# Kernel tuning notes

Hardware: AMD Instinct MI355X
Metric: run time of the kernel (lower is better)

## Reference

```python
import jax, jax.numpy as jnp
import numpy as np
import math

N_HEADS = 16
D_MODEL = 1024
DK = D_MODEL // N_HEADS
B, S = 2, 2048


def setup_inputs() -> dict:
    key = jax.random.key(0)
    ks = jax.random.split(key, 11)
    scale_in = 1.0 / math.sqrt(D_MODEL)
    scale_o = 1.0 / math.sqrt(N_HEADS * DK)
    return {
        "query": jax.random.normal(ks[0], (B, S, D_MODEL), jnp.float32),
        "key": jax.random.normal(ks[1], (B, S, D_MODEL), jnp.float32),
        "value": jax.random.normal(ks[2], (B, S, D_MODEL), jnp.float32),
        # stacked per-head projection weights [H, d_model, dk], biases [H, dk]
        "Wq": jax.random.normal(ks[3], (N_HEADS, D_MODEL, DK), jnp.float32) * scale_in,
        "bq": jax.random.normal(ks[4], (N_HEADS, DK), jnp.float32) * scale_in,
        "Wk": jax.random.normal(ks[5], (N_HEADS, D_MODEL, DK), jnp.float32) * scale_in,
        "bk": jax.random.normal(ks[6], (N_HEADS, DK), jnp.float32) * scale_in,
        "Wv": jax.random.normal(ks[7], (N_HEADS, D_MODEL, DK), jnp.float32) * scale_in,
        "bv": jax.random.normal(ks[8], (N_HEADS, DK), jnp.float32) * scale_in,
        "Wo": jax.random.normal(ks[9], (N_HEADS * DK, D_MODEL), jnp.float32) * scale_o,
        "bo": jax.random.normal(ks[10], (D_MODEL,), jnp.float32) * scale_o,
    }


def reference(query, key, value, Wq, bq, Wk, bk, Wv, bv, Wo, bo):
    # Per-head linear projections, vectorized over heads: [B,H,S,dk]
    q = jnp.einsum("bsd,hdk->bhsk", query, Wq) + bq[None, :, None, :]
    k = jnp.einsum("bsd,hdk->bhsk", key, Wk) + bk[None, :, None, :]
    v = jnp.einsum("bsd,hdk->bhsk", value, Wv) + bv[None, :, None, :]
    # Scaled dot-product scores [B,H,S,S]
    scores = jnp.einsum("bhsk,bhtk->bhst", q, k) / jnp.sqrt(jnp.asarray(DK, q.dtype))
    # FAITHFUL to source: nn.Softmax(dim=0) -> softmax over the BATCH axis
    attn = jax.nn.softmax(scores, axis=0)
    out = jnp.einsum("bhst,bhtk->bhsk", attn, v)  # [B,H,S,dk]
    # concat heads along feature dim (torch.cat dim=2)
    concat = out.transpose(0, 2, 1, 3).reshape(query.shape[0], query.shape[1], N_HEADS * DK)
    return concat @ Wo + bo
```

## Files before the change

### kernel.cpp

```cpp
#include <hip/hip_runtime.h>
#include <hip/hip_bf16.h>

#define B_ 2
#define S_ 2048
#define D_ 1024
#define H_ 16
#define DK_ 64
#define BS_ (B_ * S_)

typedef unsigned int u32;
typedef unsigned short u16;
typedef __attribute__((ext_vector_type(8))) short bf16x8;
typedef __attribute__((ext_vector_type(4))) float f32x4;

typedef const __attribute__((address_space(1))) void glb_cv;
typedef __attribute__((address_space(3))) void lds_v;

__device__ __forceinline__ void async_cp16(const void* g, void* l) {
    __builtin_amdgcn_global_load_lds((glb_cv*)g, (lds_v*)l, 16, 0, 0);
}

__device__ __forceinline__ float bf2f(u16 v) {
    union { u32 u; float f; } c; c.u = ((u32)v) << 16; return c.f;
}
__device__ __forceinline__ u16 f2bf(float f) {
    union { float f; u32 u; } c; c.f = f;
    u32 u = c.u;
    return (u16)((u + 0x7fffu + ((u >> 16) & 1u)) >> 16);
}
__device__ __forceinline__ u32 pack2(float a, float b) {
    return (u32)f2bf(a) | ((u32)f2bf(b) << 16);
}
__device__ __forceinline__ u32 packtr(float lo, float hi) {
    union { float f; u32 u; } a, b; a.f = lo; b.f = hi;
    return __builtin_amdgcn_perm(b.u, a.u, 0x07060302u);
}
__device__ __forceinline__ int sw64(int r, int c8) { return (((c8) + (r)) & 7) * 8; }

struct PrepArgs {
    const float* W[4]; u16* WT[4];
    const float* X[3]; u16* XB[3];
    float* csums;
};
__global__ __launch_bounds__(256) void prep(PrepArgs a)
{
    const int id = blockIdx.x;
    const int tid = threadIdx.x;
    if (id >= 1024) {
        const int cid = id - 1024;
        const int z = cid >> 11;
        const size_t base = (size_t)(cid & 2047) * 2048 + tid * 8;
        const float* X = a.X[z];
        float4 x0 = *(const float4*)(X + base);
        float4 x1 = *(const float4*)(X + base + 4);
        uint4 o;
        o.x = pack2(x0.x, x0.y); o.y = pack2(x0.z, x0.w);
        o.z = pack2(x1.x, x1.y); o.w = pack2(x1.z, x1.w);
        *(uint4*)(a.XB[z] + base) = o;
        return;
    }
    if (id == 0) {
        float4 zz = {0.f, 0.f, 0.f, 0.f};
        *(float4*)(a.csums + tid * 4) = zz;
    }
    __shared__ __attribute__((aligned(16))) u16 T[64][72];
    const int z = id >> 8;
    const int rem = id & 255;
    const float* W = a.W[z];
    u16* WT = a.WT[z];
    const int headMode = (z < 3) ? 1 : 0;
    const int k0 = (rem >> 4) * 64;
    const int n0 = (rem & 15) * 64;
    const int kr = tid >> 4;
    const int n4 = (tid & 15) * 4;
    #pragma unroll
    for (int pass = 0; pass < 4; ++pass) {
        int kk = k0 + pass * 16 + kr;
        const float* p = headMode
            ? (W + (size_t)((n0 + n4) >> 6) * (1024 * 64) + kk * 64 + ((n0 + n4) & 63))
            : (W + (size_t)kk * 1024 + n0 + n4);
        float4 v = *(const float4*)p;
        int krel = pass * 16 + kr;
        T[n4 + 0][krel] = f2bf(v.x);
        T[n4 + 1][krel] = f2bf(v.y);
        T[n4 + 2][krel] = f2bf(v.z);
        T[n4 + 3][krel] = f2bf(v.w);
    }
    __syncthreads();
    const int nr = tid >> 2;
    const int kq = (tid & 3) * 16;
    uint4 o0 = *(const uint4*)&T[nr][kq];
    uint4 o1 = *(const uint4*)&T[nr][kq + 8];
    u16* q = WT + (size_t)(n0 + nr) * 1024 + k0 + kq;
    *(uint4*)q = o0;
    *(uint4*)(q + 8) = o1;
}

__global__ __launch_bounds__(256) void vprep(
    const u16* __restrict__ Vb, u16* __restrict__ VT, float* __restrict__ csums)
{
    __shared__ __attribute__((aligned(16))) u16 T[64][72];
    __shared__ float red[256];
    const int tid = threadIdx.x;
    const int t0 = blockIdx.x * 64;
    const int bh = blockIdx.y;
    const int b = bh >> 4, h = bh & 15;
    const int tr = tid >> 4;
    const int d4 = (tid & 15) * 4;
    #pragma unroll
    for (int pass = 0; pass < 4; ++pass) {
        int tt = t0 + pass * 16 + tr;
        const u16* p = Vb + (size_t)(b * S_ + tt) * 1024 + h * 64 + d4;
        u32 a = *(const u32*)p;
        u32 c = *(const u32*)(p + 2);
        int trel = pass * 16 + tr;
        T[d4 + 0][trel] = (u16)a;
        T[d4 + 1][trel] = (u16)(a >> 16);
        T[d4 + 2][trel] = (u16)c;
        T[d4 + 3][trel] = (u16)(c >> 16);
    }
    __syncthreads();
    const int dr = tid >> 2;
    const int tq = (tid & 3) * 16;
    uint4 o0 = *(const uint4*)&T[dr][tq];
    uint4 o1 = *(const uint4*)&T[dr][tq + 8];
    u16* q = VT + ((size_t)bh * 64 + dr) * 2048 + t0 + tq;
    *(uint4*)q = o0;
    *(uint4*)(q + 8) = o1;

    if (b == 1) {
        const int dk = tid & 63, part = tid >> 6;
        float s = 0.f;
        #pragma unroll
        for (int t = 0; t < 16; ++t) s += bf2f(T[dk][part * 16 + t]);
        red[tid] = s;
        __syncthreads();
        if (tid < 64)
            atomicAdd(&csums[h * 64 + tid],
                      red[tid] + red[tid + 64] + red[tid + 128] + red[tid + 192]);
    }
}

struct ProjArgs {
    const u16* X[3];
    const u16* W[3];
    const float* bias[3];
    u16* Y[3];
};
__global__ __launch_bounds__(256) void proj3(ProjArgs pa)
{
    __shared__ __attribute__((aligned(16))) u16 As[128][32];
    __shared__ __attribute__((aligned(16))) u16 Bs[128][32];
    const int z = blockIdx.z;
    const u16* X = pa.X[z];
    const u16* WT = pa.W[z];
    const float* bias = pa.bias[z];
    u16* Y = pa.Y[z];
    const int neg = (z == 1);

    const int tid = threadIdx.x;
    const int lane = tid & 63;
    const int wave = tid >> 6;
    const int quad = lane >> 4;
    const int l16 = lane & 15;
    const int m0 = blockIdx.x * 128;
    const int n0 = blockIdx.y * 128;
    const int wm = (wave & 1) * 64, wn = (wave >> 1) * 64;

    f32x4 acc[4][4] = {};

    for (int k0 = 0; k0 < 1024; k0 += 32) {
        __syncthreads();
        #pragma unroll
        for (int call = 0; call < 2; ++call) {
            const int c = tid + call * 256;
            const int row = c >> 2, cc = (c & 3) * 8;
            char* la = (char*)&As[0][0] + (size_t)(c & ~63) * 16;
            async_cp16(X + (size_t)(m0 + row) * 1024 + k0 + cc, la);
            char* lb = (char*)&Bs[0][0] + (size_t)(c & ~63) * 16;
            async_cp16(WT + (size_t)(n0 + row) * 1024 + k0 + cc, lb);
        }
        __syncthreads();

        bf16x8 af[4], bfr[4];
        #pragma unroll
        for (int mt = 0; mt < 4; ++mt)
            af[mt] = *(const bf16x8*)&As[wm + mt * 16 + l16][quad * 8];
        #pragma unroll
        for (int nt = 0; nt < 4; ++nt)
            bfr[nt] = *(const bf16x8*)&Bs[wn + nt * 16 + l16][quad * 8];
        #pragma unroll
        for (int mt = 0; mt < 4; ++mt)
            #pragma unroll
            for (int nt = 0; nt < 4; ++nt)
                acc[mt][nt] = __builtin_amdgcn_mfma_f32_16x16x32_bf16(
                    af[mt], bfr[nt], acc[mt][nt], 0, 0, 0);
    }

    #pragma unroll
    for (int nt = 0; nt < 4; ++nt) {
        const int col = n0 + wn + nt * 16 + l16;
        const float bv = bias[col];
        #pragma unroll
        for (int mt = 0; mt < 4; ++mt) {
            #pragma unroll
            for (int r = 0; r < 4; ++r) {
                const int row = m0 + wm + mt * 16 + quad * 4 + r;
                float v = acc[mt][nt][r] + bv;
                if (neg && row >= 2048) v = -v;
                Y[(size_t)row * 1024 + col] = f2bf(v);
            }
        }
    }
}

__global__ __launch_bounds__(256) void gemm_out(
    const u16* __restrict__ X, const u16* __restrict__ WT,
    const float* __restrict__ bias, float* __restrict__ Y)
{
    __shared__ __attribute__((aligned(16))) u16 As[128][32];
    __shared__ __attribute__((aligned(16))) u16 Bs[64][32];
    const int tid = threadIdx.x;
    const int lane = tid & 63;
    const int wave = tid >> 6;
    const int quad = lane >> 4;
    const int l16 = lane & 15;
    const int m0 = blockIdx.x * 128;
    const int n0 = blockIdx.y * 64;
    const int wm = (wave & 1) * 64, wn = (wave >> 1) * 32;

    f32x4 acc[4][2] = {};

    for (int k0 = 0; k0 < 1024; k0 += 32) {
        __syncthreads();
        #pragma unroll
        for (int call = 0; call < 2; ++call) {
            const int c = tid + call * 256;
            const int row = c >> 2, cc = (c & 3) * 8;
            char* la = (char*)&As[0][0] + (size_t)(c & ~63) * 16;
            async_cp16(X + (size_t)(m0 + row) * 1024 + k0 + cc, la);
        }
        {
            const int c = tid;
            const int row = c >> 2, cc = (c & 3) * 8;
            char* lb = (char*)&Bs[0][0] + (size_t)(c & ~63) * 16;
            async_cp16(WT + (size_t)(n0 + row) * 1024 + k0 + cc, lb);
        }
        __syncthreads();

        bf16x8 af[4], bfr[2];
        #pragma unroll
        for (int mt = 0; mt < 4; ++mt)
            af[mt] = *(const bf16x8*)&As[wm + mt * 16 + l16][quad * 8];
        #pragma unroll
        for (int nt = 0; nt < 2; ++nt)
            bfr[nt] = *(const bf16x8*)&Bs[wn + nt * 16 + l16][quad * 8];
        #pragma unroll
        for (int mt = 0; mt < 4; ++mt)
            #pragma unroll
            for (int nt = 0; nt < 2; ++nt)
                acc[mt][nt] = __builtin_amdgcn_mfma_f32_16x16x32_bf16(
                    af[mt], bfr[nt], acc[mt][nt], 0, 0, 0);
    }

    #pragma unroll
    for (int nt = 0; nt < 2; ++nt) {
        const int col = n0 + wn + nt * 16 + l16;
        const float bv = bias[col];
        #pragma unroll
        for (int mt = 0; mt < 4; ++mt) {
            #pragma unroll
            for (int r = 0; r < 4; ++r) {
                const int row = m0 + wm + mt * 16 + quad * 4 + r;
                Y[(size_t)row * 1024 + col] = acc[mt][nt][r] + bv;
            }
        }
    }
}

__global__ __launch_bounds__(256) void attn_mfma(
    const u16* __restrict__ Qb, const u16* __restrict__ Kb,
    const u16* __restrict__ VT, const float* __restrict__ csums,
    u16* __restrict__ Cc)
{
    __shared__ __attribute__((aligned(16))) u16 Ks[2][64][64];
    __shared__ __attribute__((aligned(16))) u16 Vs[2][64][64];
    __shared__ __attribute__((aligned(16))) u16 Ps[64][64];

    const int id = blockIdx.x;
    const int xcd = id & 7, j = id >> 3;
    const int h = xcd + 8 * (j >> 5);
    const int s0 = (j & 31) * 64;

    const int tid = threadIdx.x;
    const int lane = tid & 63;
    const int wave = tid >> 6;
    const int quad = lane >> 4;
    const int l16 = lane & 15;
    const int sw = wave * 16;

    const int r_ = tid >> 2;
    const int cq = (tid & 3) * 16;
    const int cq8 = (tid & 3) * 2;

    bf16x8 qf[2][2];
    #pragma unroll
    for (int b = 0; b < 2; ++b)
        #pragma unroll
        for (int ks = 0; ks < 2; ++ks)
            qf[b][ks] = *(const bf16x8*)(Qb + (size_t)(b * S_ + s0 + sw + l16) * 1024
                                          + h * 64 + ks * 32 + quad * 8);

    f32x4 O0[4] = {}, T1[4] = {};

    for (int t0 = 0; t0 < S_; t0 += 64) {
        __syncthreads();
        #pragma unroll
        for (int b = 0; b < 2; ++b) {
            const u16* pk = Kb + (size_t)(b * S_ + t0 + r_) * 1024 + h * 64 + cq;
            *(uint4*)&Ks[b][r_][sw64(r_, cq8)]     = *(const uint4*)pk;
            *(uint4*)&Ks[b][r_][sw64(r_, cq8 + 1)] = *(const uint4*)(pk + 8);
            const u16* pv = VT + ((size_t)(b * H_ + h) * 64 + r_) * 2048 + t0 + cq;
            *(uint4*)&Vs[b][r_][sw64(r_, cq8)]     = *(const uint4*)pv;
            *(uint4*)&Vs[b][r_][sw64(r_, cq8 + 1)] = *(const uint4*)(pv + 8);
        }
        __syncthreads();

        f32x4 dacc[4] = {};
        #pragma unroll
        for (int mt = 0; mt < 4; ++mt) {
            const int kr = mt * 16 + l16;
            #pragma unroll
            for (int ks = 0; ks < 2; ++ks) {
                bf16x8 k0f = *(const bf16x8*)&Ks[0][kr][sw64(kr, ks * 4 + quad)];
                dacc[mt] = __builtin_amdgcn_mfma_f32_16x16x32_bf16(k0f, qf[0][ks], dacc[mt], 0, 0, 0);
                bf16x8 k1f = *(const bf16x8*)&Ks[1][kr][sw64(kr, ks * 4 + quad)];
                dacc[mt] = __builtin_amdgcn_mfma_f32_16x16x32_bf16(k1f, qf[1][ks], dacc[mt], 0, 0, 0);
            }
        }
        const int pr = sw + l16;
        #pragma unroll
        for (int mt = 0; mt < 4; ++mt) {
            float p[4];
            #pragma unroll
            for (int r = 0; r < 4; ++r) {
                float e = __expf(dacc[mt][r] * -0.125f);
                p[r] = __builtin_amdgcn_rcpf(1.0f + e);
            }
            uint2 w;
            w.x = packtr(p[0], p[1]);
            w.y = packtr(p[2], p[3]);
            const int c8 = 2 * mt + (quad >> 1);
            *(uint2*)&Ps[pr][sw64(pr, c8) + (quad & 1) * 4] = w;
        }
        bf16x8 pf0 = *(const bf16x8*)&Ps[pr][sw64(pr, quad)];
        bf16x8 pf1 = *(const bf16x8*)&Ps[pr][sw64(pr, 4 + quad)];
        #pragma unroll
        for (int nt = 0; nt < 4; ++nt) {
            const int vr = nt * 16 + l16;
            bf16x8 v00 = *(const bf16x8*)&Vs[0][vr][sw64(vr, quad)];
            bf16x8 v01 = *(const bf16x8*)&Vs[0][vr][sw64(vr, 4 + quad)];
            O0[nt] = __builtin_amdgcn_mfma_f32_16x16x32_bf16(pf0, v00, O0[nt], 0, 0, 0);
            O0[nt] = __builtin_amdgcn_mfma_f32_16x16x32_bf16(pf1, v01, O0[nt], 0, 0, 0);
            bf16x8 v10 = *(const bf16x8*)&Vs[1][vr][sw64(vr, quad)];
            bf16x8 v11 = *(const bf16x8*)&Vs[1][vr][sw64(vr, 4 + quad)];
            T1[nt] = __builtin_amdgcn_mfma_f32_16x16x32_bf16(pf0, v10, T1[nt], 0, 0, 0);
            T1[nt] = __builtin_amdgcn_mfma_f32_16x16x32_bf16(pf1, v11, T1[nt], 0, 0, 0);
        }
    }

    #pragma unroll
    for (int nt = 0; nt < 4; ++nt) {
        const int dk = nt * 16 + l16;
        const float cs1 = csums[h * 64 + dk];
        #pragma unroll
        for (int r = 0; r < 4; ++r) {
            const int s = s0 + sw + quad * 4 + r;
            Cc[(size_t)(0 * S_ + s) * 1024 + h * 64 + dk] = f2bf(O0[nt][r]);
            Cc[(size_t)(1 * S_ + s) * 1024 + h * 64 + dk] = f2bf(cs1 - T1[nt][r]);
        }
    }
}

extern "C" void kernel_launch(void* const* d_in, const int* in_sizes, int n_in,
                              void* d_out, int out_size, void* d_ws, size_t ws_size,
                              hipStream_t stream) {
    const float* q  = (const float*)d_in[0];
    const float* k  = (const float*)d_in[1];
    const float* v  = (const float*)d_in[2];
    const float* Wq = (const float*)d_in[3];
    const float* bq = (const float*)d_in[4];
    const float* Wk = (const float*)d_in[5];
    const float* bk = (const float*)d_in[6];
    const float* Wv = (const float*)d_in[7];
    const float* bv = (const float*)d_in[8];
    const float* Wo = (const float*)d_in[9];
    const float* bo = (const float*)d_in[10];

    char* ws = (char*)d_ws;
    const size_t MB = 1024 * 1024;
    u16* Cc  = (u16*)(ws);
    u16* Xq  = (u16*)(ws);
    u16* WqT = (u16*)(ws + 8  * MB);
    u16* WkT = (u16*)(ws + 10 * MB);
    u16* WvT = (u16*)(ws + 12 * MB);
    u16* WoT = (u16*)(ws + 14 * MB);
    u16* Qp  = (u16*)(ws + 16 * MB);
    u16* Kp  = (u16*)(ws + 24 * MB);
    u16* Vp  = (u16*)(ws + 32 * MB);
    u16* VTv = (u16*)(ws + 40 * MB);
    u16* Xk  = (u16*)(ws + 40 * MB);
    u16* Xv  = (u16*)(ws + 48 * MB);
    float* csums = (float*)d_out;

    dim3 blk(256);

    PrepArgs pr;
    pr.W[0] = Wq; pr.W[1] = Wk; pr.W[2] = Wv; pr.W[3] = Wo;
    pr.WT[0] = WqT; pr.WT[1] = WkT; pr.WT[2] = WvT; pr.WT[3] = WoT;
    pr.X[0] = q; pr.X[1] = k; pr.X[2] = v;
    pr.XB[0] = Xq; pr.XB[1] = Xk; pr.XB[2] = Xv;
    pr.csums = csums;
    prep<<<dim3(1024 + 6144), blk, 0, stream>>>(pr);

    ProjArgs pa;
    pa.X[0] = Xq; pa.X[1] = Xk; pa.X[2] = Xv;
    pa.W[0] = WqT; pa.W[1] = WkT; pa.W[2] = WvT;
    pa.bias[0] = bq; pa.bias[1] = bk; pa.bias[2] = bv;
    pa.Y[0] = Qp; pa.Y[1] = Kp; pa.Y[2] = Vp;
    proj3<<<dim3(32, 8, 3), blk, 0, stream>>>(pa);

    vprep<<<dim3(32, 32), blk, 0, stream>>>(Vp, VTv, csums);
    attn_mfma<<<dim3(512), blk, 0, stream>>>(Qp, Kp, VTv, csums, Cc);
    gemm_out<<<dim3(32, 16), blk, 0, stream>>>(Cc, WoT, bo, (float*)d_out);
}
```

Before: 233.7 us.

## Split attention key range across blocks, double-buffer K/V, merge partials in output GEMM

The attention kernel now handles 128 query rows per block and splits the key dimension into two halves across blocks. K/V tiles are staged asynchronously into double-buffered LDS, with MFMA priority hints. Each half writes its own partial output, and the column sums of V are computed inside attention instead of through atomics in vprep. The output GEMM loads both partials, adds them, applies the csum correction for batch 1, and packs the result into LDS. This trades asynchronous A loads in gemm_out for synchronous loads plus extra arithmetic, and it doubles the partial-output traffic, in exchange for more parallelism and overlap in attention.

```diff
diff --git a/kernel.cpp b/kernel.cpp
--- a/kernel.cpp
+++ b/kernel.cpp
@@ -40,7 +40,6 @@
 struct PrepArgs {
     const float* W[4]; u16* WT[4];
     const float* X[3]; u16* XB[3];
-    float* csums;
 };
 __global__ __launch_bounds__(256) void prep(PrepArgs a)
 {
@@ -58,10 +57,6 @@
         o.z = pack2(x1.x, x1.y); o.w = pack2(x1.z, x1.w);
         *(uint4*)(a.XB[z] + base) = o;
         return;
-    }
-    if (id == 0) {
-        float4 zz = {0.f, 0.f, 0.f, 0.f};
-        *(float4*)(a.csums + tid * 4) = zz;
     }
     __shared__ __attribute__((aligned(16))) u16 T[64][72];
     const int z = id >> 8;
@@ -97,10 +92,9 @@
 }
 
 __global__ __launch_bounds__(256) void vprep(
-    const u16* __restrict__ Vb, u16* __restrict__ VT, float* __restrict__ csums)
+    const u16* __restrict__ Vb, u16* __restrict__ VT)
 {
     __shared__ __attribute__((aligned(16))) u16 T[64][72];
-    __shared__ float red[256];
     const int tid = threadIdx.x;
     const int t0 = blockIdx.x * 64;
     const int bh = blockIdx.y;
@@ -127,18 +121,6 @@
     u16* q = VT + ((size_t)bh * 64 + dr) * 2048 + t0 + tq;
     *(uint4*)q = o0;
     *(uint4*)(q + 8) = o1;
-
-    if (b == 1) {
-        const int dk = tid & 63, part = tid >> 6;
-        float s = 0.f;
-        #pragma unroll
-        for (int t = 0; t < 16; ++t) s += bf2f(T[dk][part * 16 + t]);
-        red[tid] = s;
-        __syncthreads();
-        if (tid < 64)
-            atomicAdd(&csums[h * 64 + tid],
-                      red[tid] + red[tid + 64] + red[tid + 128] + red[tid + 192]);
-    }
 }
 
 struct ProjArgs {
@@ -215,8 +197,10 @@
 }
 
 __global__ __launch_bounds__(256) void gemm_out(
-    const u16* __restrict__ X, const u16* __restrict__ WT,
-    const float* __restrict__ bias, float* __restrict__ Y)
+    const u16* __restrict__ P0, const u16* __restrict__ P1,
+    const float* __restrict__ csP,
+    const u16* __restrict__ WT, const float* __restrict__ bias,
+    float* __restrict__ Y)
 {
     __shared__ __attribute__((aligned(16))) u16 As[128][32];
     __shared__ __attribute__((aligned(16))) u16 Bs[64][32];
@@ -229,23 +213,51 @@
     const int n0 = blockIdx.y * 64;
     const int wm = (wave & 1) * 64, wn = (wave >> 1) * 32;
 
+    const int arow = tid >> 1;
+    const int acol = (tid & 1) * 16;
+    const size_t abase = (size_t)(m0 + arow) * 1024;
+    const bool hiB = (m0 >= 2048);
+
     f32x4 acc[4][2] = {};
 
     for (int k0 = 0; k0 < 1024; k0 += 32) {
         __syncthreads();
-        #pragma unroll
-        for (int call = 0; call < 2; ++call) {
-            const int c = tid + call * 256;
-            const int row = c >> 2, cc = (c & 3) * 8;
-            char* la = (char*)&As[0][0] + (size_t)(c & ~63) * 16;
-            async_cp16(X + (size_t)(m0 + row) * 1024 + k0 + cc, la);
-        }
         {
             const int c = tid;
             const int row = c >> 2, cc = (c & 3) * 8;
             char* lb = (char*)&Bs[0][0] + (size_t)(c & ~63) * 16;
             async_cp16(WT + (size_t)(n0 + row) * 1024 + k0 + cc, lb);
         }
+        const size_t off = abase + k0 + acol;
+        bf16x8 a0 = *(const bf16x8*)(P0 + off);
+        bf16x8 a1 = *(const bf16x8*)(P0 + off + 8);
+        bf16x8 b0 = *(const bf16x8*)(P1 + off);
+        bf16x8 b1 = *(const bf16x8*)(P1 + off + 8);
+        float va[16];
+        #pragma unroll
+        for (int jj = 0; jj < 8; ++jj) {
+            va[jj]     = bf2f((u16)a0[jj]) + bf2f((u16)b0[jj]);
+            va[8 + jj] = bf2f((u16)a1[jj]) + bf2f((u16)b1[jj]);
+        }
+        if (hiB) {
+            #pragma unroll
+            for (int g = 0; g < 4; ++g) {
+                const int cb = k0 + acol + g * 4;
+                float4 c0 = *(const float4*)(csP + cb);
+                float4 c1 = *(const float4*)(csP + 1024 + cb);
+                va[g * 4 + 0] = (c0.x + c1.x) - va[g * 4 + 0];
+                va[g * 4 + 1] = (c0.y + c1.y) - va[g * 4 + 1];
+                va[g * 4 + 2] = (c0.z + c1.z) - va[g * 4 + 2];
+                va[g * 4 + 3] = (c0.w + c1.w) - va[g * 4 + 3];
+            }
+        }
+        uint4 w0, w1;
+        w0.x = pack2(va[0], va[1]);   w0.y = pack2(va[2], va[3]);
+        w0.z = pack2(va[4], va[5]);   w0.w = pack2(va[6], va[7]);
+        w1.x = pack2(va[8], va[9]);   w1.y = pack2(va[10], va[11]);
+        w1.z = pack2(va[12], va[13]); w1.w = pack2(va[14], va[15]);
+        *(uint4*)&As[arow][acol] = w0;
+        *(uint4*)&As[arow][acol + 8] = w1;
         __syncthreads();
 
         bf16x8 af[4], bfr[2];
@@ -280,105 +292,159 @@
 
 __global__ __launch_bounds__(256) void attn_mfma(
     const u16* __restrict__ Qb, const u16* __restrict__ Kb,
-    const u16* __restrict__ VT, const float* __restrict__ csums,
-    u16* __restrict__ Cc)
+    const u16* __restrict__ VT, float* __restrict__ csP,
+    u16* __restrict__ P0, u16* __restrict__ P1)
 {
-    __shared__ __attribute__((aligned(16))) u16 Ks[2][64][64];
-    __shared__ __attribute__((aligned(16))) u16 Vs[2][64][64];
-    __shared__ __attribute__((aligned(16))) u16 Ps[64][64];
+    __shared__ __attribute__((aligned(16))) u16 Ks[2][2][64][64];
+    __shared__ __attribute__((aligned(16))) u16 Vs[2][2][64][64];
+    __shared__ __attribute__((aligned(16))) u16 Ps[128][64];
 
     const int id = blockIdx.x;
-    const int xcd = id & 7, j = id >> 3;
-    const int h = xcd + 8 * (j >> 5);
-    const int s0 = (j & 31) * 64;
+    const int xcd = id & 7;
+    const int rj = id >> 3;
+    const int h = xcd * 2 + (rj >> 5);
+    const int half = (rj >> 4) & 1;
+    const int st = rj & 15;
+    const int s0 = st * 128;
+    const int tbase = half * 1024;
+    u16* Pout = half ? P1 : P0;
 
     const int tid = threadIdx.x;
     const int lane = tid & 63;
     const int wave = tid >> 6;
     const int quad = lane >> 4;
     const int l16 = lane & 15;
-    const int sw = wave * 16;
-
-    const int r_ = tid >> 2;
-    const int cq = (tid & 3) * 16;
-    const int cq8 = (tid & 3) * 2;
-
-    bf16x8 qf[2][2];
+    const int sr8 = lane >> 3;
+    const int sc8 = lane & 7;
+
+    auto stage = [&](int buf, int t0) {
+        #pragma unroll
+        for (int c = 0; c < 4; ++c) {
+            const int kc = c * 4 + wave;
+            const int bb = kc >> 3, row0 = (kc & 7) * 8;
+            const int rr = row0 + sr8;
+            const int cg = (sc8 - rr) & 7;
+            async_cp16(Kb + (size_t)(bb * S_ + tbase + t0 + rr) * 1024 + h * 64 + cg * 8,
+                       &Ks[buf][bb][row0][0]);
+            async_cp16(VT + ((size_t)(bb * H_ + h) * 64 + rr) * 2048 + tbase + t0 + cg * 8,
+                       &Vs[buf][bb][row0][0]);
+        }
+    };
+
+    bf16x8 qf[2][2][2];
     #pragma unroll
-    for (int b = 0; b < 2; ++b)
-        #pragma unroll
-        for (int ks = 0; ks < 2; ++ks)
-            qf[b][ks] = *(const bf16x8*)(Qb + (size_t)(b * S_ + s0 + sw + l16) * 1024
-                                          + h * 64 + ks * 32 + quad * 8);
-
-    f32x4 O0[4] = {}, T1[4] = {};
-
-    for (int t0 = 0; t0 < S_; t0 += 64) {
-        __syncthreads();
-        #pragma unroll
-        for (int b = 0; b < 2; ++b) {
-            const u16* pk = Kb + (size_t)(b * S_ + t0 + r_) * 1024 + h * 64 + cq;
-            *(uint4*)&Ks[b][r_][sw64(r_, cq8)]     = *(const uint4*)pk;
-            *(uint4*)&Ks[b][r_][sw64(r_, cq8 + 1)] = *(const uint4*)(pk + 8);
-            const u16* pv = VT + ((size_t)(b * H_ + h) * 64 + r_) * 2048 + t0 + cq;
-            *(uint4*)&Vs[b][r_][sw64(r_, cq8)]     = *(const uint4*)pv;
-            *(uint4*)&Vs[b][r_][sw64(r_, cq8 + 1)] = *(const uint4*)(pv + 8);
-        }
-        __syncthreads();
-
-        f32x4 dacc[4] = {};
+    for (int sg = 0; sg < 2; ++sg)
+        #pragma unroll
+        for (int b = 0; b < 2; ++b)
+            #pragma unroll
+            for (int ks = 0; ks < 2; ++ks)
+                qf[sg][b][ks] = *(const bf16x8*)(Qb
+                    + (size_t)(b * S_ + s0 + wave * 32 + sg * 16 + l16) * 1024
+                    + h * 64 + ks * 32 + quad * 8);
+
+    f32x4 O0[2][4] = {}, T1[2][4] = {};
+    float cacc = 0.f;
+
+    stage(0, 0);
+    __syncthreads();
+    int cur = 0;
+    for (int t0 = 0; t0 < 1024; t0 += 64) {
+        if (t0 + 64 < 1024) stage(cur ^ 1, t0 + 64);
+
+        f32x4 dacc[2][4] = {};
+        __builtin_amdgcn_s_setprio(1);
         #pragma unroll
         for (int mt = 0; mt < 4; ++mt) {
             const int kr = mt * 16 + l16;
             #pragma unroll
             for (int ks = 0; ks < 2; ++ks) {
-                bf16x8 k0f = *(const bf16x8*)&Ks[0][kr][sw64(kr, ks * 4 + quad)];
-                dacc[mt] = __builtin_amdgcn_mfma_f32_16x16x32_bf16(k0f, qf[0][ks], dacc[mt], 0, 0, 0);
-                bf16x8 k1f = *(const bf16x8*)&Ks[1][kr][sw64(kr, ks * 4 + quad)];
-                dacc[mt] = __builtin_amdgcn_mfma_f32_16x16x32_bf16(k1f, qf[1][ks], dacc[mt], 0, 0, 0);
-            }
-        }
-        const int pr = sw + l16;
-        #pragma unroll
-        for (int mt = 0; mt < 4; ++mt) {
-            float p[4];
-            #pragma unroll
-            for (int r = 0; r < 4; ++r) {
-                float e = __expf(dacc[mt][r] * -0.125f);
-                p[r] = __builtin_amdgcn_rcpf(1.0f + e);
-            }
-            uint2 w;
-            w.x = packtr(p[0], p[1]);
-            w.y = packtr(p[2], p[3]);
-            const int c8 = 2 * mt + (quad >> 1);
-            *(uint2*)&Ps[pr][sw64(pr, c8) + (quad & 1) * 4] = w;
-        }
-        bf16x8 pf0 = *(const bf16x8*)&Ps[pr][sw64(pr, quad)];
-        bf16x8 pf1 = *(const bf16x8*)&Ps[pr][sw64(pr, 4 + quad)];
+                bf16x8 k0f = *(const bf16x8*)&Ks[cur][0][kr][sw64(kr, ks * 4 + quad)];
+                bf16x8 k1f = *(const bf16x8*)&Ks[cur][1][kr][sw64(kr, ks * 4 + quad)];
+                #pragma unroll
+                for (int sg = 0; sg < 2; ++sg) {
+                    dacc[sg][mt] = __builtin_amdgcn_mfma_f32_16x16x32_bf16(
+                        k0f, qf[sg][0][ks], dacc[sg][mt], 0, 0, 0);
+                    dacc[sg][mt] = __builtin_amdgcn_mfma_f32_16x16x32_bf16(
+                        k1f, qf[sg][1][ks], dacc[sg][mt], 0, 0, 0);
+                }
+            }
+        }
+        __builtin_amdgcn_s_setprio(0);
+
+        #pragma unroll
+        for (int sg = 0; sg < 2; ++sg) {
+            const int pr = wave * 32 + sg * 16 + l16;
+            #pragma unroll
+            for (int mt = 0; mt < 4; ++mt) {
+                float p[4];
+                #pragma unroll
+                for (int rr = 0; rr < 4; ++rr) {
+                    float e = __expf(dacc[sg][mt][rr] * -0.125f);
+                    p[rr] = __builtin_amdgcn_rcpf(1.0f + e);
+                }
+                uint2 w;
+                w.x = packtr(p[0], p[1]);
+                w.y = packtr(p[2], p[3]);
+                const int c8 = 2 * mt + (quad >> 1);
+                *(uint2*)&Ps[pr][sw64(pr, c8) + (quad & 1) * 4] = w;
+            }
+        }
+
+        if (st == 0) {
+            const int dk = tid >> 2, tp = tid & 3;
+            bf16x8 vA = *(const bf16x8*)&Vs[cur][1][dk][sw64(dk, tp * 2)];
+            bf16x8 vB = *(const bf16x8*)&Vs[cur][1][dk][sw64(dk, tp * 2 + 1)];
+            #pragma unroll
+            for (int jj = 0; jj < 8; ++jj)
+                cacc += bf2f((u16)vA[jj]) + bf2f((u16)vB[jj]);
+        }
+
+        bf16x8 pf[2][2];
+        #pragma unroll
+        for (int sg = 0; sg < 2; ++sg) {
+            const int pr = wave * 32 + sg * 16 + l16;
+            pf[sg][0] = *(const bf16x8*)&Ps[pr][sw64(pr, quad)];
+            pf[sg][1] = *(const bf16x8*)&Ps[pr][sw64(pr, 4 + quad)];
+        }
+        __builtin_amdgcn_s_setprio(1);
         #pragma unroll
         for (int nt = 0; nt < 4; ++nt) {
             const int vr = nt * 16 + l16;
-            bf16x8 v00 = *(const bf16x8*)&Vs[0][vr][sw64(vr, quad)];
-            bf16x8 v01 = *(const bf16x8*)&Vs[0][vr][sw64(vr, 4 + quad)];
-            O0[nt] = __builtin_amdgcn_mfma_f32_16x16x32_bf16(pf0, v00, O0[nt], 0, 0, 0);
-            O0[nt] = __builtin_amdgcn_mfma_f32_16x16x32_bf16(pf1, v01, O0[nt], 0, 0, 0);
-            bf16x8 v10 = *(const bf16x8*)&Vs[1][vr][sw64(vr, quad)];
-            bf16x8 v11 = *(const bf16x8*)&Vs[1][vr][sw64(vr, 4 + quad)];
-            T1[nt] = __builtin_amdgcn_mfma_f32_16x16x32_bf16(pf0, v10, T1[nt], 0, 0, 0);
-            T1[nt] = __builtin_amdgcn_mfma_f32_16x16x32_bf16(pf1, v11, T1[nt], 0, 0, 0);
-        }
+            bf16x8 v00 = *(const bf16x8*)&Vs[cur][0][vr][sw64(vr, quad)];
+            bf16x8 v01 = *(const bf16x8*)&Vs[cur][0][vr][sw64(vr, 4 + quad)];
+            bf16x8 v10 = *(const bf16x8*)&Vs[cur][1][vr][sw64(vr, quad)];
+            bf16x8 v11 = *(const bf16x8*)&Vs[cur][1][vr][sw64(vr, 4 + quad)];
+            #pragma unroll
+            for (int sg = 0; sg < 2; ++sg) {
+                O0[sg][nt] = __builtin_amdgcn_mfma_f32_16x16x32_bf16(pf[sg][0], v00, O0[sg][nt], 0, 0, 0);
+                O0[sg][nt] = __builtin_amdgcn_mfma_f32_16x16x32_bf16(pf[sg][1], v01, O0[sg][nt], 0, 0, 0);
+                T1[sg][nt] = __builtin_amdgcn_mfma_f32_16x16x32_bf16(pf[sg][0], v10, T1[sg][nt], 0, 0, 0);
+                T1[sg][nt] = __builtin_amdgcn_mfma_f32_16x16x32_bf16(pf[sg][1], v11, T1[sg][nt], 0, 0, 0);
+            }
+        }
+        __builtin_amdgcn_s_setprio(0);
+        __syncthreads();
+        cur ^= 1;
     }
 
     #pragma unroll
-    for (int nt = 0; nt < 4; ++nt) {
-        const int dk = nt * 16 + l16;
-        const float cs1 = csums[h * 64 + dk];
-        #pragma unroll
-        for (int r = 0; r < 4; ++r) {
-            const int s = s0 + sw + quad * 4 + r;
-            Cc[(size_t)(0 * S_ + s) * 1024 + h * 64 + dk] = f2bf(O0[nt][r]);
-            Cc[(size_t)(1 * S_ + s) * 1024 + h * 64 + dk] = f2bf(cs1 - T1[nt][r]);
-        }
+    for (int sg = 0; sg < 2; ++sg)
+        #pragma unroll
+        for (int nt = 0; nt < 4; ++nt) {
+            const int dk = nt * 16 + l16;
+            #pragma unroll
+            for (int rr = 0; rr < 4; ++rr) {
+                const int s = s0 + wave * 32 + sg * 16 + quad * 4 + rr;
+                Pout[(size_t)(0 * S_ + s) * 1024 + h * 64 + dk] = f2bf(O0[sg][nt][rr]);
+                Pout[(size_t)(1 * S_ + s) * 1024 + h * 64 + dk] = f2bf(T1[sg][nt][rr]);
+            }
+        }
+
+    if (st == 0) {
+        cacc += __shfl_xor(cacc, 1);
+        cacc += __shfl_xor(cacc, 2);
+        if ((tid & 3) == 0)
+            csP[half * 1024 + h * 64 + (tid >> 2)] = cacc;
     }
 }
 
@@ -399,8 +465,8 @@
 
     char* ws = (char*)d_ws;
     const size_t MB = 1024 * 1024;
-    u16* Cc  = (u16*)(ws);
     u16* Xq  = (u16*)(ws);
+    float* csP = (float*)(ws);
     u16* WqT = (u16*)(ws + 8  * MB);
     u16* WkT = (u16*)(ws + 10 * MB);
     u16* WvT = (u16*)(ws + 12 * MB);
@@ -408,10 +474,11 @@
     u16* Qp  = (u16*)(ws + 16 * MB);
     u16* Kp  = (u16*)(ws + 24 * MB);
     u16* Vp  = (u16*)(ws + 32 * MB);
+    u16* Pa  = (u16*)(ws + 32 * MB);
     u16* VTv = (u16*)(ws + 40 * MB);
     u16* Xk  = (u16*)(ws + 40 * MB);
     u16* Xv  = (u16*)(ws + 48 * MB);
-    float* csums = (float*)d_out;
+    u16* Pb  = (u16*)(ws + 48 * MB);
 
     dim3 blk(256);
 
@@ -420,7 +487,6 @@
     pr.WT[0] = WqT; pr.WT[1] = WkT; pr.WT[2] = WvT; pr.WT[3] = WoT;
     pr.X[0] = q; pr.X[1] = k; pr.X[2] = v;
     pr.XB[0] = Xq; pr.XB[1] = Xk; pr.XB[2] = Xv;
-    pr.csums = csums;
     prep<<<dim3(1024 + 6144), blk, 0, stream>>>(pr);
 
     ProjArgs pa;
@@ -430,7 +496,7 @@
     pa.Y[0] = Qp; pa.Y[1] = Kp; pa.Y[2] = Vp;
     proj3<<<dim3(32, 8, 3), blk, 0, stream>>>(pa);
 
-    vprep<<<dim3(32, 32), blk, 0, stream>>>(Vp, VTv, csums);
-    attn_mfma<<<dim3(512), blk, 0, stream>>>(Qp, Kp, VTv, csums, Cc);
-    gemm_out<<<dim3(32, 16), blk, 0, stream>>>(Cc, WoT, bo, (float*)d_out);
-}
+    vprep<<<dim3(32, 32), blk, 0, stream>>>(Vp, VTv);
+    attn_mfma<<<dim3(512), blk, 0, stream>>>(Qp, Kp, VTv, csP, Pa, Pb);
+    gemm_out<<<dim3(32, 16), blk, 0, stream>>>(Pa, Pb, csP, WoT, bo, (float*)d_out);
+}
```

Measured after the change: 249.4 us. 6.7% more time.
